# Kernel tuning notes

Measured on AMD Instinct MI355X. Metric: run time of the kernel, lower is better.

## Reference

```python
import jax, jax.numpy as jnp
import numpy as np

B, T, C = 2, 2048, 1024
NUM_HEADS, QK_LEN, V_LEN = 16, 64, 64


def setup_inputs() -> dict:
    key = jax.random.key(0)
    ks = jax.random.split(key, 11)
    s = 0.02
    return {
        "Q": jax.random.normal(ks[0], (B, T, C), jnp.float32),
        "K": jax.random.normal(ks[1], (B, T, C), jnp.float32),
        "V": jax.random.normal(ks[2], (B, T, C), jnp.float32),
        # Linear weights stored as (in, out); y = x @ W + b
        "Wq": jax.random.normal(ks[3], (C, NUM_HEADS * QK_LEN), jnp.float32) * s,
        "bq": jnp.zeros((NUM_HEADS * QK_LEN,), jnp.float32),
        "Wk": jax.random.normal(ks[4], (C, NUM_HEADS * QK_LEN), jnp.float32) * s,
        "bk": jnp.zeros((NUM_HEADS * QK_LEN,), jnp.float32),
        "Wv": jax.random.normal(ks[5], (C, NUM_HEADS * V_LEN), jnp.float32) * s,
        "bv": jnp.zeros((NUM_HEADS * V_LEN,), jnp.float32),
        "Wo": jax.random.normal(ks[6], (NUM_HEADS * V_LEN, C), jnp.float32) * s,
        "bo": jnp.zeros((C,), jnp.float32),
    }


def _split_heads(x, n_heads, d):
    b, t, _ = x.shape
    return x.reshape(b, t, n_heads, d).transpose(0, 2, 1, 3)  # (B,H,T,d)


def reference(Q, K, V, Wq, bq, Wk, bk, Wv, bv, Wo, bo):
    q = _split_heads(Q @ Wq + bq, NUM_HEADS, QK_LEN)   # (B,H,T,dk)
    k = _split_heads(K @ Wk + bk, NUM_HEADS, QK_LEN)   # (B,H,T,dk)
    v = _split_heads(V @ Wv + bv, NUM_HEADS, V_LEN)    # (B,H,T,dv)

    scale = 1.0 / jnp.sqrt(jnp.asarray(QK_LEN, q.dtype))
    scores = jnp.einsum("bhqd,bhkd->bhqk", q, k) * scale  # (B,H,T,T)
    attn = jax.nn.softmax(scores, axis=-1)
    out = jnp.einsum("bhqk,bhkd->bhqd", attn, v)           # (B,H,T,dv)

    out = out.transpose(0, 2, 1, 3).reshape(Q.shape[0], Q.shape[1], NUM_HEADS * V_LEN)
    return out @ Wo + bo
```

## Files before the change

### kernel.cpp

```cpp
#include <hip/hip_runtime.h>
#include <hip/hip_bf16.h>
#include <math.h>

constexpr int B = 2, T = 2048, C = 1024, H = 16, D = 64;
constexpr int M = B * T;
constexpr float SCALE_L2E = 0.125f * 1.4426950408889634f;

typedef __attribute__((ext_vector_type(8))) short s16x8;
typedef __attribute__((ext_vector_type(4))) short s16x4;
typedef __attribute__((ext_vector_type(4))) float fv4;

typedef unsigned short ushort_t;

static __device__ __forceinline__ ushort_t f2bf(float x) {
    union { float f; unsigned u; } c; c.f = x;
    unsigned u = c.u + 0x7FFFu + ((c.u >> 16) & 1u);
    return (ushort_t)(u >> 16);
}

static __device__ __forceinline__ int cvt_pk_bf16(float lo, float hi) {
    int r;
    asm("v_cvt_pk_bf16_f32 %0, %1, %2" : "=v"(r) : "v"(lo), "v"(hi));
    return r;
}

#define GLDS(gp, lp) __builtin_amdgcn_global_load_lds( \
    (const __attribute__((address_space(1))) void*)(gp), \
    (__attribute__((address_space(3))) void*)(lp), 16, 0, 0)

__global__ __launch_bounds__(256) void prep(
    const float* __restrict__ Q, const float* __restrict__ K,
    const float* __restrict__ V,
    const float* __restrict__ W0, const float* __restrict__ W1,
    const float* __restrict__ W2, const float* __restrict__ W3,
    ushort_t* __restrict__ dst, ushort_t* __restrict__ Wt)
{
    __shared__ ushort_t tile[64][72];
    const int tid = threadIdx.x;

    if (blockIdx.x < 6144) {
        size_t e = ((size_t)blockIdx.x * 256 + tid) * 8;
        const float* src;
        size_t base;
        if (e < (size_t)M * C)          { src = Q; base = 0; }
        else if (e < 2 * (size_t)M * C) { src = K; base = (size_t)M * C; }
        else                            { src = V; base = 2 * (size_t)M * C; }
        const float* p = src + (e - base);
        float4 a = *(const float4*)p;
        float4 b = *(const float4*)(p + 4);
        union { s16x8 v; int i[4]; } o;
        o.i[0] = cvt_pk_bf16(a.x, a.y);
        o.i[1] = cvt_pk_bf16(a.z, a.w);
        o.i[2] = cvt_pk_bf16(b.x, b.y);
        o.i[3] = cvt_pk_bf16(b.z, b.w);
        *(s16x8*)(dst + e) = o.v;
        return;
    }

    const int idx = blockIdx.x - 6144;
    const int s = idx >> 8;
    const float* W = (s == 0) ? W0 : (s == 1) ? W1 : (s == 2) ? W2 : W3;
    const int k0 = (idx & 15) * 64, n0 = ((idx >> 4) & 15) * 64;
#pragma unroll
    for (int it = 0; it < 4; it++) {
        int f = it * 256 + tid;
        int r = f >> 4, c4 = (f & 15) * 4;
        float4 x = *(const float4*)(W + (size_t)(k0 + r) * C + n0 + c4);
        *(int*)&tile[r][c4]     = cvt_pk_bf16(x.x, x.y);
        *(int*)&tile[r][c4 + 2] = cvt_pk_bf16(x.z, x.w);
    }
    __syncthreads();
#pragma unroll
    for (int it = 0; it < 4; it++) {
        int f = it * 256 + tid;
        int rr = f >> 4, c4 = (f & 15) * 4;
        union { s16x4 v; ushort_t u[4]; } u;
#pragma unroll
        for (int j = 0; j < 4; j++) u.u[j] = tile[c4 + j][rr];
        *(s16x4*)(Wt + (size_t)(s * 1024 + n0 + rr) * 1024 + k0 + c4) = u.v;
    }
}

__global__ __launch_bounds__(256) void gemm_qkv(
    const ushort_t* __restrict__ qkv, const ushort_t* __restrict__ Wt,
    const float* __restrict__ bq, const float* __restrict__ bk,
    const float* __restrict__ bv,
    ushort_t* __restrict__ qw, ushort_t* __restrict__ kw,
    ushort_t* __restrict__ vt)
{
    __shared__ ushort_t sm[17408];
    ushort_t* As0 = sm;
    ushort_t* Bs0 = sm + 8192;

    const int tid = threadIdx.x;
    const int w = tid >> 6, lane = tid & 63;
    const int quad = lane >> 4, lc = lane & 15;
    const int wm = w & 1, wn = w >> 1;

    const int lin = blockIdx.y * 24 + blockIdx.x;
    const int xcd = lin % 8;
    const int i_ = lin / 8;
    const int s = i_ >> 5;
    const int r_ = i_ & 31;
    const int m0 = (xcd * 4 + (r_ >> 3)) * 128;
    const int nt = s * 8 + (r_ & 7);
    const int nsec0 = (nt & 7) * 128;

    const ushort_t* Abase = qkv + (size_t)s * M * C;
    const ushort_t* Btbase = Wt + (size_t)nt * 128 * 1024;

    const int srow = (w << 4) + (lane >> 2);
    const int ske  = (lane & 3) * 8;

    fv4 acc[4][4] = {};

    auto stage = [&](int k0, int buf) {
#pragma unroll
        for (int i = 0; i < 2; i++) {
            int row = i * 64 + srow;
            GLDS(Abase + (size_t)(m0 + row) * 1024 + k0 + ske,
                 As0 + buf * 4096 + i * 2048 + w * 512);
            GLDS(Btbase + (size_t)row * 1024 + k0 + ske,
                 Bs0 + buf * 4096 + i * 2048 + w * 512);
        }
    };

    stage(0, 0);
    __syncthreads();

    for (int k0 = 0; k0 < 1024; k0 += 32) {
        const int cur = (k0 >> 5) & 1;
        if (k0 + 32 < 1024) stage(k0 + 32, cur ^ 1);

        s16x8 af[4], bf[4];
#pragma unroll
        for (int ms = 0; ms < 4; ms++)
            af[ms] = *(const s16x8*)(As0 + cur * 4096 + (wm * 64 + ms * 16 + lc) * 32 + quad * 8);
#pragma unroll
        for (int ns = 0; ns < 4; ns++)
            bf[ns] = *(const s16x8*)(Bs0 + cur * 4096 + (wn * 64 + ns * 16 + lc) * 32 + quad * 8);
#pragma unroll
        for (int ms = 0; ms < 4; ms++)
#pragma unroll
            for (int ns = 0; ns < 4; ns++)
                acc[ms][ns] = __builtin_amdgcn_mfma_f32_16x16x32_bf16(
                    af[ms], bf[ns], acc[ms][ns], 0, 0, 0);
        __syncthreads();
    }

    if (s == 2) {
        ushort_t* tp = sm;
#pragma unroll
        for (int ns = 0; ns < 4; ns++) {
            const int nl = wn * 64 + ns * 16 + lc;
            const float bias = bv[nsec0 + nl];
#pragma unroll
            for (int ms = 0; ms < 4; ms++) {
                const int ml = wm * 64 + ms * 16 + quad * 4;
                union { s16x4 v; int i2[2]; } u;
                u.i2[0] = cvt_pk_bf16(acc[ms][ns][0] + bias, acc[ms][ns][1] + bias);
                u.i2[1] = cvt_pk_bf16(acc[ms][ns][2] + bias, acc[ms][ns][3] + bias);
                *(s16x4*)&tp[nl * 136 + ml] = u.v;
            }
        }
        __syncthreads();
        const int b_ = m0 >> 11, t0 = m0 & 2047;
#pragma unroll
        for (int it = 0; it < 8; it++) {
            const int row = it * 16 + (tid >> 4);
            const int ch = tid & 15;
            const int n = nsec0 + row;
            const int h_ = n >> 6, d_ = n & 63;
            s16x8 v8 = *(const s16x8*)&tp[row * 136 + ch * 8];
            *(s16x8*)(vt + ((size_t)(b_ * H + h_) * 64 + d_) * T + t0 + ch * 8) = v8;
        }
        return;
    }

    const float* biasp = (s == 0) ? bq : bk;
    const float premul = (s == 0) ? SCALE_L2E : 1.0f;
    ushort_t* outp = (s == 0) ? qw : kw;

#pragma unroll
    for (int ns = 0; ns < 4; ns++) {
        const int nl = nsec0 + wn * 64 + ns * 16 + lc;
        const float bias = biasp[nl];
        const int h_ = nl >> 6, d_ = nl & 63;
#pragma unroll
        for (int ms = 0; ms < 4; ms++) {
#pragma unroll
            for (int r = 0; r < 4; r++) {
                int m = m0 + wm * 64 + ms * 16 + quad * 4 + r;
                float val = (acc[ms][ns][r] + bias) * premul;
                int b_ = m >> 11, t_ = m & (T - 1);
                size_t bh = (size_t)(b_ * H + h_);
                outp[((bh * T + t_) << 6) + d_] = f2bf(val);
            }
        }
    }
}

__global__ __launch_bounds__(256) void gemm_final(
    const ushort_t* __restrict__ A, const ushort_t* __restrict__ Wot,
    const float* __restrict__ bo, float* __restrict__ out)
{
    __shared__ ushort_t As[2][128 * 32];
    __shared__ ushort_t Bs[2][64 * 32];

    const int tid = threadIdx.x;
    const int w = tid >> 6, lane = tid & 63;
    const int quad = lane >> 4, lc = lane & 15;
    const int wm = w & 1, wn = w >> 1;

    const int lin = blockIdx.y * 16 + blockIdx.x;
    const int xcd = lin & 7;
    const int i_ = lin >> 3;
    const int m0 = (xcd * 4 + (i_ >> 4)) * 128;
    const int n0 = (i_ & 15) * 64;

    const int srow = (w << 4) + (lane >> 2);
    const int ske  = (lane & 3) * 8;

    fv4 acc[4][2] = {};

    auto stage = [&](int k0, int buf) {
        GLDS(A + (size_t)(m0 + srow) * 1024 + k0 + ske,      As[buf] + w * 512);
        GLDS(A + (size_t)(m0 + 64 + srow) * 1024 + k0 + ske, As[buf] + 2048 + w * 512);
        GLDS(Wot + (size_t)(n0 + srow) * 1024 + k0 + ske,    Bs[buf] + w * 512);
    };

    stage(0, 0);
    __syncthreads();

    for (int k0 = 0; k0 < 1024; k0 += 32) {
        const int cur = (k0 >> 5) & 1;
        if (k0 + 32 < 1024) stage(k0 + 32, cur ^ 1);

        s16x8 af[4], bf[2];
#pragma unroll
        for (int ms = 0; ms < 4; ms++)
            af[ms] = *(const s16x8*)(As[cur] + (wm * 64 + ms * 16 + lc) * 32 + quad * 8);
#pragma unroll
        for (int ns = 0; ns < 2; ns++)
            bf[ns] = *(const s16x8*)(Bs[cur] + (wn * 32 + ns * 16 + lc) * 32 + quad * 8);
#pragma unroll
        for (int ms = 0; ms < 4; ms++)
#pragma unroll
            for (int ns = 0; ns < 2; ns++)
                acc[ms][ns] = __builtin_amdgcn_mfma_f32_16x16x32_bf16(
                    af[ms], bf[ns], acc[ms][ns], 0, 0, 0);
        __syncthreads();
    }

#pragma unroll
    for (int ns = 0; ns < 2; ns++) {
        const int n = n0 + wn * 32 + ns * 16 + lc;
        const float bias = bo[n];
#pragma unroll
        for (int ms = 0; ms < 4; ms++) {
#pragma unroll
            for (int r = 0; r < 4; r++) {
                int m = m0 + wm * 64 + ms * 16 + quad * 4 + r;
                out[(size_t)m * 1024 + n] = acc[ms][ns][r] + bias;
            }
        }
    }
}

__global__ __launch_bounds__(256, 4) void attn(
    const ushort_t* __restrict__ q, const ushort_t* __restrict__ k,
    const ushort_t* __restrict__ vT, ushort_t* __restrict__ o)
{
    __shared__ alignas(16) ushort_t ks[2][64 * 64];
    __shared__ alignas(16) ushort_t vs[2][64 * 64];

    const int tid = threadIdx.x;
    const int w = tid >> 6, lane = tid & 63;
    const int quad = lane >> 4, lc = lane & 15;
    const int cs = lc & 7;
    const int qsub = w & 1, ksub = w >> 1;

    const int id = blockIdx.y * 32 + blockIdx.x;
    const int qt = (id >> 3) & 31;
    const int bh = (id & 7) * 4 + (id >> 8);

    s16x8 aq[2][2];
    const ushort_t* qb = q + ((size_t)bh * T + qt * 64 + qsub * 32) * D;
#pragma unroll
    for (int j = 0; j < 2; j++)
#pragma unroll
        for (int h = 0; h < 2; h++)
            aq[j][h] = *(const s16x8*)(qb + (size_t)(j * 16 + lc) * D + h * 32 + quad * 8);

    fv4 accO[2][4] = {};
    float psum[2] = {0.f, 0.f};

    const ushort_t* kb0 = k + (size_t)bh * T * D;
    const ushort_t* vb0 = vT + (size_t)bh * D * T;

    const int sr8 = lane >> 3;
    const int sch = (lane & 7) ^ sr8;

    auto stage = [&](int kt, int buf) {
#pragma unroll
        for (int i = 0; i < 2; i++) {
            const int r = w * 16 + i * 8 + sr8;
            GLDS(kb0 + (size_t)(kt * 64 + r) * 64 + sch * 8,
                 ks[buf] + (w * 16 + i * 8) * 64);
            GLDS(vb0 + (size_t)r * T + kt * 64 + sch * 8,
                 vs[buf] + (w * 16 + i * 8) * 64);
        }
    };

    stage(0, 0);
    __syncthreads();

    for (int kt = 0; kt < T / 64; kt++) {
        const int cur = kt & 1;
        if (kt + 1 < T / 64) stage(kt + 1, cur ^ 1);

        fv4 accST[2][2] = {};
        __builtin_amdgcn_s_setprio(1);
#pragma unroll
        for (int t4k = 0; t4k < 2; t4k++) {
            const int row = ksub * 32 + t4k * 16 + lc;
            s16x8 ak0 = *(const s16x8*)(ks[cur] + row * 64 + ((quad ^ cs) << 3));
            s16x8 ak1 = *(const s16x8*)(ks[cur] + row * 64 + (((quad + 4) ^ cs) << 3));
#pragma unroll
            for (int j = 0; j < 2; j++) {
                accST[j][t4k] = __builtin_amdgcn_mfma_f32_16x16x32_bf16(
                    ak0, aq[j][0], accST[j][t4k], 0, 0, 0);
                accST[j][t4k] = __builtin_amdgcn_mfma_f32_16x16x32_bf16(
                    ak1, aq[j][1], accST[j][t4k], 0, 0, 0);
            }
        }
        __builtin_amdgcn_s_setprio(0);

        s16x8 av[4];
#pragma unroll
        for (int t4v = 0; t4v < 4; t4v++) {
            const int row = t4v * 16 + lc;
            av[t4v] = *(const s16x8*)(vs[cur] + row * 64 + (((ksub * 4 + quad) ^ cs) << 3));
        }

#pragma unroll
        for (int j = 0; j < 2; j++) {
            float p0 = __builtin_amdgcn_exp2f(accST[j][0][0]);
            float p1 = __builtin_amdgcn_exp2f(accST[j][0][1]);
            float p2 = __builtin_amdgcn_exp2f(accST[j][0][2]);
            float p3 = __builtin_amdgcn_exp2f(accST[j][0][3]);
            float p4 = __builtin_amdgcn_exp2f(accST[j][1][0]);
            float p5 = __builtin_amdgcn_exp2f(accST[j][1][1]);
            float p6 = __builtin_amdgcn_exp2f(accST[j][1][2]);
            float p7 = __builtin_amdgcn_exp2f(accST[j][1][3]);
            psum[j] += ((p0 + p1) + (p2 + p3)) + ((p4 + p5) + (p6 + p7));

            int W00 = cvt_pk_bf16(p0, p1);
            int W01 = cvt_pk_bf16(p2, p3);
            int W10 = cvt_pk_bf16(p4, p5);
            int W11 = cvt_pk_bf16(p6, p7);
            asm("v_permlane32_swap_b32 %0, %1" : "+v"(W00), "+v"(W10));
            asm("v_permlane16_swap_b32 %0, %1" : "+v"(W00), "+v"(W10));
            asm("v_permlane32_swap_b32 %0, %1" : "+v"(W01), "+v"(W11));
            asm("v_permlane16_swap_b32 %0, %1" : "+v"(W01), "+v"(W11));

            union { int i[4]; s16x8 v; } pbu;
            pbu.i[0] = W00; pbu.i[1] = W01; pbu.i[2] = W10; pbu.i[3] = W11;

            __builtin_amdgcn_s_setprio(1);
#pragma unroll
            for (int t4v = 0; t4v < 4; t4v++)
                accO[j][t4v] = __builtin_amdgcn_mfma_f32_16x16x32_bf16(
                    av[t4v], pbu.v, accO[j][t4v], 0, 0, 0);
            __builtin_amdgcn_s_setprio(0);
        }

        __syncthreads();
    }

#pragma unroll
    for (int j = 0; j < 2; j++) {
        psum[j] += __shfl_xor(psum[j], 16);
        psum[j] += __shfl_xor(psum[j], 32);
    }

    float* sc = (float*)&ks[0][0];
#pragma unroll
    for (int c = 0; c < 4; c++) {
        const int j = c >> 1, tv = (c & 1) * 2;
        __syncthreads();
        if (ksub == 1) {
            *(fv4*)(sc + ((qsub * 64 + lane) * 8))     = accO[j][tv];
            *(fv4*)(sc + ((qsub * 64 + lane) * 8 + 4)) = accO[j][tv + 1];
        }
        __syncthreads();
        if (ksub == 0) {
            accO[j][tv]     += *(fv4*)(sc + ((qsub * 64 + lane) * 8));
            accO[j][tv + 1] += *(fv4*)(sc + ((qsub * 64 + lane) * 8 + 4));
        }
    }
    __syncthreads();
    if (ksub == 1) {
        sc[(qsub * 64 + lane) * 2]     = psum[0];
        sc[(qsub * 64 + lane) * 2 + 1] = psum[1];
    }
    __syncthreads();
    if (ksub == 0) {
        psum[0] += sc[(qsub * 64 + lane) * 2];
        psum[1] += sc[(qsub * 64 + lane) * 2 + 1];

        const int b_ = bh >> 4, h_ = bh & 15;
#pragma unroll
        for (int j = 0; j < 2; j++) {
            float inv = 1.0f / psum[j];
            int row = qt * 64 + qsub * 32 + j * 16 + lc;
            ushort_t* op = o + ((size_t)b_ * T + row) * C + h_ * 64;
#pragma unroll
            for (int t4v = 0; t4v < 4; t4v++) {
                union { s16x4 v; int i[2]; } u;
                u.i[0] = cvt_pk_bf16(accO[j][t4v][0] * inv, accO[j][t4v][1] * inv);
                u.i[1] = cvt_pk_bf16(accO[j][t4v][2] * inv, accO[j][t4v][3] * inv);
                *(s16x4*)(op + t4v * 16 + quad * 4) = u.v;
            }
        }
    }
}

extern "C" void kernel_launch(void* const* d_in, const int* in_sizes, int n_in,
                              void* d_out, int out_size, void* d_ws, size_t ws_size,
                              hipStream_t stream)
{
    const float* Q  = (const float*)d_in[0];
    const float* K  = (const float*)d_in[1];
    const float* V  = (const float*)d_in[2];
    const float* Wq = (const float*)d_in[3];
    const float* bq = (const float*)d_in[4];
    const float* Wk = (const float*)d_in[5];
    const float* bk = (const float*)d_in[6];
    const float* Wv = (const float*)d_in[7];
    const float* bv = (const float*)d_in[8];
    const float* Wo = (const float*)d_in[9];
    const float* bo = (const float*)d_in[10];
    float* out = (float*)d_out;

    ushort_t* qkvbf = (ushort_t*)d_ws;
    ushort_t* Wt = qkvbf + (size_t)3 * M * C;
    ushort_t* qw = Wt + (size_t)4096 * 1024;
    ushort_t* kw = qw + (size_t)M * C;
    ushort_t* vt = kw + (size_t)M * C;
    ushort_t* ow = qkvbf;
    ushort_t* Wot = Wt + (size_t)3072 * 1024;

    dim3 blk(256);
    prep<<<dim3(7168), blk, 0, stream>>>(Q, K, V, Wq, Wk, Wv, Wo, qkvbf, Wt);
    gemm_qkv<<<dim3(24, 32), blk, 0, stream>>>(qkvbf, Wt, bq, bk, bv, qw, kw, vt);
    attn<<<dim3(T / 64, B * H), blk, 0, stream>>>(qw, kw, vt, ow);
    gemm_final<<<dim3(16, 32), blk, 0, stream>>>(ow, Wot, bo, out);
}
```

Before: 221.9 us.

## Fuse fp32-to-bf16 activation conversion into QKV GEMM A-tile loading

Removes the separate conversion pass over Q, K, V in the prep kernel. The QKV GEMM now loads fp32 activations into registers, converts them to bf16, and writes them to LDS while the current tile's MFMAs run. This eliminates a full read-and-write pass over the activations. In exchange, each GEMM block re-reads fp32 data (twice the bytes) for every N tile and needs more registers.

Result: slower. 262.7 us (+18.4%).

```diff
diff --git a/kernel.cpp b/kernel.cpp
--- a/kernel.cpp
+++ b/kernel.cpp
@@ -29,35 +29,13 @@
     (__attribute__((address_space(3))) void*)(lp), 16, 0, 0)
 
 __global__ __launch_bounds__(256) void prep(
-    const float* __restrict__ Q, const float* __restrict__ K,
-    const float* __restrict__ V,
     const float* __restrict__ W0, const float* __restrict__ W1,
     const float* __restrict__ W2, const float* __restrict__ W3,
-    ushort_t* __restrict__ dst, ushort_t* __restrict__ Wt)
+    ushort_t* __restrict__ Wt)
 {
     __shared__ ushort_t tile[64][72];
     const int tid = threadIdx.x;
-
-    if (blockIdx.x < 6144) {
-        size_t e = ((size_t)blockIdx.x * 256 + tid) * 8;
-        const float* src;
-        size_t base;
-        if (e < (size_t)M * C)          { src = Q; base = 0; }
-        else if (e < 2 * (size_t)M * C) { src = K; base = (size_t)M * C; }
-        else                            { src = V; base = 2 * (size_t)M * C; }
-        const float* p = src + (e - base);
-        float4 a = *(const float4*)p;
-        float4 b = *(const float4*)(p + 4);
-        union { s16x8 v; int i[4]; } o;
-        o.i[0] = cvt_pk_bf16(a.x, a.y);
-        o.i[1] = cvt_pk_bf16(a.z, a.w);
-        o.i[2] = cvt_pk_bf16(b.x, b.y);
-        o.i[3] = cvt_pk_bf16(b.z, b.w);
-        *(s16x8*)(dst + e) = o.v;
-        return;
-    }
-
-    const int idx = blockIdx.x - 6144;
+    const int idx = blockIdx.x;
     const int s = idx >> 8;
     const float* W = (s == 0) ? W0 : (s == 1) ? W1 : (s == 2) ? W2 : W3;
     const int k0 = (idx & 15) * 64, n0 = ((idx >> 4) & 15) * 64;
@@ -82,7 +60,8 @@
 }
 
 __global__ __launch_bounds__(256) void gemm_qkv(
-    const ushort_t* __restrict__ qkv, const ushort_t* __restrict__ Wt,
+    const float* __restrict__ Qf, const float* __restrict__ Kf,
+    const float* __restrict__ Vf, const ushort_t* __restrict__ Wt,
     const float* __restrict__ bq, const float* __restrict__ bk,
     const float* __restrict__ bv,
     ushort_t* __restrict__ qw, ushort_t* __restrict__ kw,
@@ -106,31 +85,55 @@
     const int nt = s * 8 + (r_ & 7);
     const int nsec0 = (nt & 7) * 128;
 
-    const ushort_t* Abase = qkv + (size_t)s * M * C;
+    const float* Af = (s == 0) ? Qf : (s == 1) ? Kf : Vf;
     const ushort_t* Btbase = Wt + (size_t)nt * 128 * 1024;
 
     const int srow = (w << 4) + (lane >> 2);
     const int ske  = (lane & 3) * 8;
 
+    const int ar = tid >> 1;
+    const int ah = (tid & 1) * 16;
+    const float* apb = Af + (size_t)(m0 + ar) * 1024 + ah;
+
     fv4 acc[4][4] = {};
 
-    auto stage = [&](int k0, int buf) {
+    auto stageB = [&](int k0, int buf) {
 #pragma unroll
         for (int i = 0; i < 2; i++) {
             int row = i * 64 + srow;
-            GLDS(Abase + (size_t)(m0 + row) * 1024 + k0 + ske,
-                 As0 + buf * 4096 + i * 2048 + w * 512);
             GLDS(Btbase + (size_t)row * 1024 + k0 + ske,
                  Bs0 + buf * 4096 + i * 2048 + w * 512);
         }
     };
-
-    stage(0, 0);
+    float4 areg[4];
+    auto loadA = [&](int k0) {
+        const float4* p = (const float4*)(apb + k0);
+        areg[0] = p[0]; areg[1] = p[1]; areg[2] = p[2]; areg[3] = p[3];
+    };
+    auto writeA = [&](int buf) {
+        union { s16x8 v; int i[4]; } u0, u1;
+        u0.i[0] = cvt_pk_bf16(areg[0].x, areg[0].y);
+        u0.i[1] = cvt_pk_bf16(areg[0].z, areg[0].w);
+        u0.i[2] = cvt_pk_bf16(areg[1].x, areg[1].y);
+        u0.i[3] = cvt_pk_bf16(areg[1].z, areg[1].w);
+        u1.i[0] = cvt_pk_bf16(areg[2].x, areg[2].y);
+        u1.i[1] = cvt_pk_bf16(areg[2].z, areg[2].w);
+        u1.i[2] = cvt_pk_bf16(areg[3].x, areg[3].y);
+        u1.i[3] = cvt_pk_bf16(areg[3].z, areg[3].w);
+        ushort_t* dst = As0 + buf * 4096 + ar * 32 + ah;
+        *(s16x8*)dst = u0.v;
+        *(s16x8*)(dst + 8) = u1.v;
+    };
+
+    stageB(0, 0);
+    loadA(0);
+    writeA(0);
     __syncthreads();
 
     for (int k0 = 0; k0 < 1024; k0 += 32) {
         const int cur = (k0 >> 5) & 1;
-        if (k0 + 32 < 1024) stage(k0 + 32, cur ^ 1);
+        const bool pf = (k0 + 32 < 1024);
+        if (pf) { stageB(k0 + 32, cur ^ 1); loadA(k0 + 32); }
 
         s16x8 af[4], bf[4];
 #pragma unroll
@@ -145,6 +148,8 @@
             for (int ns = 0; ns < 4; ns++)
                 acc[ms][ns] = __builtin_amdgcn_mfma_f32_16x16x32_bf16(
                     af[ms], bf[ns], acc[ms][ns], 0, 0, 0);
+
+        if (pf) writeA(cur ^ 1);
         __syncthreads();
     }
 
@@ -443,17 +448,16 @@
     const float* bo = (const float*)d_in[10];
     float* out = (float*)d_out;
 
-    ushort_t* qkvbf = (ushort_t*)d_ws;
-    ushort_t* Wt = qkvbf + (size_t)3 * M * C;
+    ushort_t* ow = (ushort_t*)d_ws;
+    ushort_t* Wt = ow + (size_t)3 * M * C;
     ushort_t* qw = Wt + (size_t)4096 * 1024;
     ushort_t* kw = qw + (size_t)M * C;
     ushort_t* vt = kw + (size_t)M * C;
-    ushort_t* ow = qkvbf;
     ushort_t* Wot = Wt + (size_t)3072 * 1024;
 
     dim3 blk(256);
-    prep<<<dim3(7168), blk, 0, stream>>>(Q, K, V, Wq, Wk, Wv, Wo, qkvbf, Wt);
-    gemm_qkv<<<dim3(24, 32), blk, 0, stream>>>(qkvbf, Wt, bq, bk, bv, qw, kw, vt);
+    prep<<<dim3(1024), blk, 0, stream>>>(Wq, Wk, Wv, Wo, Wt);
+    gemm_qkv<<<dim3(24, 32), blk, 0, stream>>>(Q, K, V, Wt, bq, bk, bv, qw, kw, vt);
     attn<<<dim3(T / 64, B * H), blk, 0, stream>>>(qw, kw, vt, ow);
     gemm_final<<<dim3(16, 32), blk, 0, stream>>>(ow, Wot, bo, out);
 }
```

## Double K-tile depth in output-projection GEMM with XOR-swizzled LDS layout

Applied to the files above, without the earlier changes.

The final output-projection GEMM now stages 64-wide K tiles instead of 32, which halves the number of loop iterations and block barriers. Shared-memory rows are laid out with an XOR swizzle on 16-byte chunks, both when filling LDS and when reading fragments, to avoid bank conflicts on the wider rows. LDS use per block doubles, which may lower occupancy, and each stage issues more global-to-LDS loads.

Result: no change. 221.2 us (-0.3%).

```diff
diff --git a/kernel.cpp b/kernel.cpp
--- a/kernel.cpp
+++ b/kernel.cpp
@@ -88,7 +88,7 @@
     ushort_t* __restrict__ qw, ushort_t* __restrict__ kw,
     ushort_t* __restrict__ vt)
 {
-    __shared__ ushort_t sm[17408];
+    __shared__ alignas(16) ushort_t sm[17408];
     ushort_t* As0 = sm;
     ushort_t* Bs0 = sm + 8192;
 
@@ -204,13 +204,14 @@
     const ushort_t* __restrict__ A, const ushort_t* __restrict__ Wot,
     const float* __restrict__ bo, float* __restrict__ out)
 {
-    __shared__ ushort_t As[2][128 * 32];
-    __shared__ ushort_t Bs[2][64 * 32];
+    __shared__ alignas(16) ushort_t As[2][128 * 64];
+    __shared__ alignas(16) ushort_t Bs[2][64 * 64];
 
     const int tid = threadIdx.x;
     const int w = tid >> 6, lane = tid & 63;
     const int quad = lane >> 4, lc = lane & 15;
     const int wm = w & 1, wn = w >> 1;
+    const int c7 = lc & 7;
 
     const int lin = blockIdx.y * 16 + blockIdx.x;
     const int xcd = lin & 7;
@@ -218,37 +219,58 @@
     const int m0 = (xcd * 4 + (i_ >> 4)) * 128;
     const int n0 = (i_ & 15) * 64;
 
-    const int srow = (w << 4) + (lane >> 2);
-    const int ske  = (lane & 3) * 8;
+    const int r8 = lane >> 3;
+    const int sch = (lane & 7) ^ r8;
 
     fv4 acc[4][2] = {};
 
     auto stage = [&](int k0, int buf) {
-        GLDS(A + (size_t)(m0 + srow) * 1024 + k0 + ske,      As[buf] + w * 512);
-        GLDS(A + (size_t)(m0 + 64 + srow) * 1024 + k0 + ske, As[buf] + 2048 + w * 512);
-        GLDS(Wot + (size_t)(n0 + srow) * 1024 + k0 + ske,    Bs[buf] + w * 512);
+#pragma unroll
+        for (int i = 0; i < 4; i++) {
+            int row = w * 32 + i * 8 + r8;
+            GLDS(A + (size_t)(m0 + row) * 1024 + k0 + sch * 8,
+                 As[buf] + (w * 32 + i * 8) * 64);
+        }
+#pragma unroll
+        for (int i = 0; i < 2; i++) {
+            int row = w * 16 + i * 8 + r8;
+            GLDS(Wot + (size_t)(n0 + row) * 1024 + k0 + sch * 8,
+                 Bs[buf] + (w * 16 + i * 8) * 64);
+        }
     };
 
     stage(0, 0);
     __syncthreads();
 
-    for (int k0 = 0; k0 < 1024; k0 += 32) {
-        const int cur = (k0 >> 5) & 1;
-        if (k0 + 32 < 1024) stage(k0 + 32, cur ^ 1);
-
-        s16x8 af[4], bf[2];
+    for (int k0 = 0; k0 < 1024; k0 += 64) {
+        const int cur = (k0 >> 6) & 1;
+        if (k0 + 64 < 1024) stage(k0 + 64, cur ^ 1);
+
+        s16x8 af[4][2], bf[2][2];
+#pragma unroll
+        for (int ms = 0; ms < 4; ms++) {
+            const int row = wm * 64 + ms * 16 + lc;
+#pragma unroll
+            for (int kh = 0; kh < 2; kh++)
+                af[ms][kh] = *(const s16x8*)(As[cur] + row * 64
+                                             + (((kh * 4 + quad) ^ c7) << 3));
+        }
+#pragma unroll
+        for (int ns = 0; ns < 2; ns++) {
+            const int row = wn * 32 + ns * 16 + lc;
+#pragma unroll
+            for (int kh = 0; kh < 2; kh++)
+                bf[ns][kh] = *(const s16x8*)(Bs[cur] + row * 64
+                                             + (((kh * 4 + quad) ^ c7) << 3));
+        }
 #pragma unroll
         for (int ms = 0; ms < 4; ms++)
-            af[ms] = *(const s16x8*)(As[cur] + (wm * 64 + ms * 16 + lc) * 32 + quad * 8);
-#pragma unroll
-        for (int ns = 0; ns < 2; ns++)
-            bf[ns] = *(const s16x8*)(Bs[cur] + (wn * 32 + ns * 16 + lc) * 32 + quad * 8);
-#pragma unroll
-        for (int ms = 0; ms < 4; ms++)
 #pragma unroll
             for (int ns = 0; ns < 2; ns++)
-                acc[ms][ns] = __builtin_amdgcn_mfma_f32_16x16x32_bf16(
-                    af[ms], bf[ns], acc[ms][ns], 0, 0, 0);
+#pragma unroll
+                for (int kh = 0; kh < 2; kh++)
+                    acc[ms][ns] = __builtin_amdgcn_mfma_f32_16x16x32_bf16(
+                        af[ms][kh], bf[ns][kh], acc[ms][ns], 0, 0, 0);
         __syncthreads();
     }
 
```
